# Performance work log

Hardware: AMD Instinct MI355X
Metric: run time of the kernel (lower is better)

The kernel has to match this reference:

```python
import jax, jax.numpy as jnp
import numpy as np

BIT = 64
NUM_TRAIN = 100000
N_CLASS = 100
BATCH = 128
MU, NU, ETA = 1.0, 1.0, 55.0
DCC_ITER = 3


def setup_inputs() -> dict:
    key = jax.random.key(0)
    k1, k2, k3, k4, k5, k6 = jax.random.split(key, 6)
    u = jax.random.normal(k1, (BATCH, BIT), dtype=jnp.float32)
    labels = jax.random.randint(k2, (BATCH,), 0, N_CLASS)
    y = jax.nn.one_hot(labels, N_CLASS, dtype=jnp.float32)          # [batch, n_class]
    U = jax.random.normal(k3, (BIT, NUM_TRAIN), dtype=jnp.float32)  # [bit, num_train]
    B = jnp.sign(jax.random.normal(k4, (BIT, NUM_TRAIN), dtype=jnp.float32))
    ylab = jax.random.randint(k5, (NUM_TRAIN,), 0, N_CLASS)
    Y = jax.nn.one_hot(ylab, N_CLASS, dtype=jnp.float32).T          # [n_class, num_train]
    ind = jax.random.randint(k6, (BATCH,), 0, NUM_TRAIN)
    return {"u": u, "y": y, "U": U, "B": B, "Y": Y, "ind": ind}


def _update_b_and_w(B, U, Y):
    """Discrete cyclic coordinate descent. Math identical to torch loop, but
    P = W@Y + eta/mu*U is hoisted out of the bit loop (W is constant there),
    and B'.T @ W' @ w (row i excluded) is computed as (W@w)@B - (w.w)*B[i]."""
    c_eye = (NU / MU) * jnp.eye(BIT, dtype=B.dtype)
    # DCC operates on sign outputs; gradients through it are zero in torch too.
    Bs = jax.lax.stop_gradient(B)
    Ys = jax.lax.stop_gradient(Y)
    Us = jax.lax.stop_gradient(U)
    B_before = Bs
    for _ in range(DCC_ITER):
        B_before = Bs
        W = jnp.linalg.inv(Bs @ Bs.T + c_eye) @ Bs @ Ys.T   # [bit, n_class]
        P = W @ Ys + (ETA / MU) * Us                        # [bit, num_train]
        def step(Bc, i):
            w = W[i]                     # [n_class]
            p = P[i]                     # [num_train]
            Ww = W @ w                   # [bit]
            full = Ww @ Bc               # [num_train]; includes row i contribution
            new_row = jnp.sign(p - (full - (w @ w) * Bc[i]))
            return Bc.at[i].set(new_row), None
        Bs, _ = jax.lax.scan(step, Bs, jnp.arange(BIT))
    # torch keeps the W computed at the START of the last dcc iteration
    # (i.e. from B before its last inner update), using the un-detached Y.
    W = jnp.linalg.inv(B_before @ B_before.T + c_eye) @ B_before @ Y.T
    return Bs, W


def reference(u, y, U, B, Y, ind):
    # in-place buffer writes: U[:, ind] = u.T.data ; Y[:, ind] = y.T
    U = U.at[:, ind].set(jax.lax.stop_gradient(u).T)
    Y = Y.at[:, ind].set(y.T)
    B, W = _update_b_and_w(B, U, Y)

    ip = (u @ U) * 0.5                           # [batch, num_train]
    s = (y @ Y > 0).astype(ip.dtype)             # [batch, num_train]
    likelihood = jnp.log1p(jnp.exp(-jnp.abs(ip))) + jnp.maximum(ip, 0.0) - s * ip
    likelihood_loss = likelihood.mean()

    cl_loss = jnp.mean((y.T - W.T @ B[:, ind]) ** 2)   # [n_class, batch]
    reg_loss = jnp.mean(W ** 2)
    return likelihood_loss + MU * cl_loss + NU * reg_loss
```

## Files before the change

kernel.cpp:

```cpp
#include <hip/hip_runtime.h>
#include <hip/hip_bf16.h>

#define NTRAIN 100000
#define NBIT   64
#define NCLASS 100
#define NBATCH 128
#define NW     1563
#define NWP    1568
#define NP1    100001.0f
#define ETA_MU 55.0f

#define NBLK   391
#define NLIKB  1563
#define NCLB   50
#define CCH    16
#define NCHUNK 98
#define SCAP   4096
#define SLACK  2e-5f

typedef unsigned long long u64;
typedef unsigned int u32;
typedef __attribute__((ext_vector_type(8))) short bf16x8;
typedef __attribute__((ext_vector_type(4))) float f32x4;

#define OFF_BMASK   0u
#define OFF_CMASK   800000u
#define OFF_LABELY  2054400u
#define OFF_OVR     2454400u
#define OFF_YLAB    2854400u
#define OFF_CCOUNT  2854912u
#define OFF_AF      2855424u
#define OFF_RHS     2871808u
#define OFF_W       2897408u
#define OFF_WT      2923008u
#define OFF_G       2948608u
#define OFF_ROWABS  2964992u
#define OFF_SCNT    2965248u
#define OFF_SLIST   2965504u
#define OFF_SOLD    2981888u
#define OFF_PA      3014656u
#define OFF_CLP     3022848u
#define OFF_PB      4620288u

__device__ __forceinline__ float blk_reduce_sum(float v, float* sbuf) {
    int tid = threadIdx.x;
    for (int off = 32; off > 0; off >>= 1) v += __shfl_down(v, off, 64);
    __syncthreads();
    if ((tid & 63) == 0) sbuf[tid >> 6] = v;
    __syncthreads();
    float t = 0.f;
    if (tid == 0) {
        int nw = (int)(blockDim.x >> 6);
        for (int q = 0; q < nw; ++q) t += sbuf[q];
    }
    return t;
}

__device__ __forceinline__ short f2bf(float v) {
    __hip_bfloat16 h = __float2bfloat16(v);
    return *reinterpret_cast<short*>(&h);
}

__global__ void k_scatter(const float* __restrict__ y, const int* __restrict__ ind,
                          int* __restrict__ ovr, int* __restrict__ ylab,
                          int* __restrict__ ccount) {
    __shared__ int cls[NBATCH], idx[NBATCH];
    int k = threadIdx.x;
    if (k < NCLASS) ccount[k] = 0;
    if (k < NBATCH) {
        int c = 0;
        for (int r = 0; r < NCLASS; ++r)
            if (y[k * NCLASS + r] > 0.5f) c = r;
        cls[k] = c; idx[k] = ind[k]; ylab[k] = c;
    }
    __syncthreads();
    if (k == 0) {
        for (int q = 0; q < NBATCH; ++q) ovr[idx[q]] = q + 1;
    }
}

__global__ __launch_bounds__(256) void k_prep(const float* __restrict__ Y,
                                              const float* __restrict__ B,
                                              const int* __restrict__ ovr,
                                              const int* __restrict__ ylab,
                                              int* __restrict__ labelY,
                                              u64* __restrict__ Bmask,
                                              u64* __restrict__ cmask,
                                              int* __restrict__ ccount) {
    __shared__ int hist[NCLASS];
    int tid = threadIdx.x, lane = tid & 63, wid = tid >> 6;
    if (tid < NCLASS) hist[tid] = 0;
    __syncthreads();
    int w = blockIdx.x * 4 + wid;
    int j = w * 64 + lane;
    int lab = -1;
    if (j < NTRAIN) {
        lab = 0;
        for (int r = 0; r < NCLASS; ++r)
            if (Y[r * NTRAIN + j] > 0.5f) lab = r;
        int ov = ovr[j];
        if (ov) lab = ylab[ov - 1];
        labelY[j] = lab;
        u64 m = 0ull;
        #pragma unroll
        for (int i = 0; i < NBIT; ++i)
            if (B[i * NTRAIN + j] > 0.0f) m |= (1ull << i);
        Bmask[j] = m;
        atomicAdd(&hist[lab], 1);
    }
    u64 keep0 = 0ull, keep1 = 0ull;
    for (int c = 0; c < NCLASS; ++c) {
        u64 bal = __ballot(lab == c);
        if (lane == c)      keep0 = bal;
        if (lane == c - 64) keep1 = bal;
    }
    if (w < NW) {
        cmask[(size_t)lane * NWP + w] = keep0;
        if (lane < NCLASS - 64) cmask[(size_t)(lane + 64) * NWP + w] = keep1;
    }
    __syncthreads();
    if (tid < NCLASS && hist[tid]) atomicAdd(&ccount[tid], hist[tid]);
}

__global__ __launch_bounds__(1024) void k_bbt4(const u64* __restrict__ Bmask,
                                               const u64* __restrict__ cmask,
                                               int* __restrict__ pA,
                                               int* __restrict__ pB) {
    __shared__ u64 Lp[64 * 17];
    __shared__ u64 Lc[100 * 17];
    int tid = threadIdx.x, lane = tid & 63, wv = tid >> 6;
    int w0 = blockIdx.x * CCH;
    for (int idx = tid; idx < 100 * CCH; idx += 1024) {
        int r = idx >> 4, w = idx & 15;
        int gw = w0 + w;
        Lc[r * 17 + w] = (gw < NW) ? cmask[(size_t)r * NWP + gw] : 0ull;
    }
    {
        int j = (w0 + wv) * 64 + lane;
        u64 m = (j < NTRAIN) ? Bmask[j] : 0ull;
        u64 acc = 0ull;
        #pragma unroll
        for (int i = 0; i < 64; ++i) {
            u64 bal = __ballot((m >> i) & 1ull);
            if (lane == i) acc = bal;
        }
        Lp[lane * 17 + wv] = acc;
    }
    __syncthreads();
    int k = lane;
    int cntA[4], cntB[7];
    #pragma unroll
    for (int i = 0; i < 4; ++i) cntA[i] = 0;
    #pragma unroll
    for (int i = 0; i < 7; ++i) cntB[i] = 0;
    #pragma unroll
    for (int w = 0; w < CCH; ++w) {
        u64 pkw = Lp[k * 17 + w];
        #pragma unroll
        for (int li = 0; li < 4; ++li)
            cntA[li] += __popcll(pkw ^ Lp[(wv + 16 * li) * 17 + w]);
        #pragma unroll
        for (int ci = 0; ci < 7; ++ci) {
            int c = wv + 16 * ci;
            if (c < NCLASS)
                cntB[ci] += __popcll(pkw & Lc[c * 17 + w]);
        }
    }
    size_t bA = (size_t)blockIdx.x * 4096;
    size_t bB = (size_t)blockIdx.x * 6400;
    #pragma unroll
    for (int li = 0; li < 4; ++li)
        pA[bA + (size_t)(wv + 16 * li) * 64 + k] = cntA[li];
    #pragma unroll
    for (int ci = 0; ci < 7; ++ci) {
        int c = wv + 16 * ci;
        if (c < NCLASS)
            pB[bB + (size_t)c * 64 + k] = cntB[ci];
    }
}

__global__ __launch_bounds__(256) void k_reduce(const int* __restrict__ pA,
                                                const int* __restrict__ pB,
                                                const int* __restrict__ ccount,
                                                float* __restrict__ A_f,
                                                float* __restrict__ RHS_f) {
    int tid = threadIdx.x, blk = blockIdx.x;
    if (blk < 16) {
        int e = blk * 256 + tid;
        int s = 0;
        #pragma unroll 4
        for (int ch = 0; ch < NCHUNK; ++ch) s += pA[(size_t)ch * 4096 + e];
        A_f[e] = ((e >> 6) == (e & 63)) ? 0.0f
                                        : (float)(NTRAIN - 2 * s) * (1.0f / NP1);
    } else {
        int e = (blk - 16) * 256 + tid;
        int s = 0;
        #pragma unroll 4
        for (int ch = 0; ch < NCHUNK; ++ch) s += pB[(size_t)ch * 6400 + e];
        RHS_f[e] = (float)(2 * s - ccount[e >> 6]);
    }
}

__global__ __launch_bounds__(256) void k_wsolve(const float* __restrict__ A_f,
                                                const float* __restrict__ RHS_f,
                                                float* __restrict__ W_g,
                                                float* __restrict__ WT_g) {
    __shared__ float As[64 * 65];
    __shared__ float xb[4][64];
    int tid = threadIdx.x, lane = tid & 63, wid = tid >> 6;
    for (int e = tid; e < 4096; e += 256)
        As[(e >> 6) * 65 + (e & 63)] = A_f[e];
    int c = blockIdx.x * 4 + wid;
    float v = RHS_f[c * 64 + lane];
    float x = v;
    __syncthreads();
    for (int it = 0; it < 4; ++it) {
        xb[wid][lane] = x;
        __syncthreads();
        const float* __restrict__ Ar = As + lane * 65;
        const float* __restrict__ xv = xb[wid];
        float a0 = 0, a1 = 0, a2 = 0, a3 = 0;
        #pragma unroll 8
        for (int k = 0; k < 64; k += 4) {
            a0 = fmaf(Ar[k],     xv[k],     a0);
            a1 = fmaf(Ar[k + 1], xv[k + 1], a1);
            a2 = fmaf(Ar[k + 2], xv[k + 2], a2);
            a3 = fmaf(Ar[k + 3], xv[k + 3], a3);
        }
        x = v - ((a0 + a1) + (a2 + a3));
        __syncthreads();
    }
    float w = x * (1.0f / NP1);
    W_g[lane * 100 + c] = w;
    WT_g[c * 64 + lane] = w;
}

__global__ __launch_bounds__(256) void k_gram(const float* __restrict__ WT,
                                              float* __restrict__ G_g,
                                              float* __restrict__ rowabs,
                                              int* __restrict__ scnt) {
    __shared__ float WTs[6400];
    int tid = threadIdx.x;
    for (int e = tid; e < 6400; e += 256) WTs[e] = WT[e];
    __syncthreads();
    int e = blockIdx.x * 256 + tid;
    int k = e >> 6, l = e & 63;
    float a0 = 0, a1 = 0;
    #pragma unroll 10
    for (int c = 0; c < 100; c += 2) {
        a0 = fmaf(WTs[c * 64 + k],       WTs[c * 64 + l],       a0);
        a1 = fmaf(WTs[(c + 1) * 64 + k], WTs[(c + 1) * 64 + l], a1);
    }
    float g = (k == l) ? 0.0f : (a0 + a1);
    G_g[e] = g;
    float v = fabsf(g);
    for (int off = 32; off > 0; off >>= 1) v += __shfl_down(v, off, 64);
    if ((tid & 63) == 0) rowabs[k] = v;
    if (blockIdx.x == 0 && tid == 0) *scnt = 0;
}

__global__ __launch_bounds__(256) void k_fast(const float* __restrict__ U,
                                              const float* __restrict__ u,
                                              const int* __restrict__ labelY,
                                              const int* __restrict__ ovr,
                                              const float* __restrict__ WT,
                                              const float* __restrict__ rowabs,
                                              u64* __restrict__ Bmask,
                                              int* __restrict__ slist,
                                              u64* __restrict__ sold,
                                              int* __restrict__ scnt) {
    __shared__ float WTs[100 * 65];
    __shared__ float ra[64];
    int tid = threadIdx.x;
    for (int e = tid; e < 6400; e += 256)
        WTs[(e >> 6) * 65 + (e & 63)] = WT[e];
    if (tid < 64) ra[tid] = rowabs[tid] + SLACK;
    __syncthreads();
    int j = blockIdx.x * 256 + tid;
    if (j >= NTRAIN) return;
    int c = labelY[j], ov = ovr[j];
    const float* up; int str;
    if (ov) { up = u + (ov - 1) * NBIT; str = 1; }
    else    { up = U + j;               str = NTRAIN; }
    const float* wc = WTs + c * 65;
    u64 m = 0ull;
    int slow = 0;
    #pragma unroll
    for (int i = 0; i < NBIT; ++i) {
        float p = fmaf(ETA_MU, up[i * str], wc[i]);
        if (p > 0.0f) m |= (1ull << i);
        slow |= (fabsf(p) <= ra[i]);
    }
    if (slow) {
        int idx = atomicAdd(scnt, 1);
        if (idx < SCAP) { slist[idx] = j; sold[idx] = Bmask[j]; }
    }
    Bmask[j] = m;
}

__global__ __launch_bounds__(1024) void k_slow(const int* __restrict__ slist,
                                               const u64* __restrict__ sold,
                                               const int* __restrict__ scnt,
                                               const int* __restrict__ labelY,
                                               const int* __restrict__ ovr,
                                               const float* __restrict__ G_g,
                                               const float* __restrict__ WT,
                                               const float* __restrict__ U,
                                               const float* __restrict__ u,
                                               u64* __restrict__ Bmask) {
    __shared__ float Gs[64 * 65];
    int tid = threadIdx.x, lane = tid & 63, wv = tid >> 6;
    int n = *scnt; if (n > SCAP) n = SCAP;
    if (n == 0) return;
    for (int e = tid; e < 4096; e += 1024)
        Gs[(e >> 6) * 65 + (e & 63)] = G_g[e];
    __syncthreads();
    for (int idx = wv; idx < n; idx += 16) {
        int j = slist[idx];
        u64 m0 = sold[idx];
        int c = labelY[j], ov = ovr[j];
        float uval = ov ? u[(ov - 1) * NBIT + lane]
                        : U[(size_t)lane * NTRAIN + j];
        float p = fmaf(ETA_MU, uval, WT[c * 64 + lane]);
        float s = ((m0 >> lane) & 1ull) ? 1.0f : -1.0f;
        for (int i = 0; i < 64; ++i) {
            float t = Gs[i * 65 + lane] * s;
            t += __shfl_xor(t, 1);  t += __shfl_xor(t, 2);
            t += __shfl_xor(t, 4);  t += __shfl_xor(t, 8);
            t += __shfl_xor(t, 16); t += __shfl_xor(t, 32);
            float nv = ((p - t) > 0.0f) ? 1.0f : -1.0f;
            s = (lane == i) ? nv : s;
        }
        u64 mo = __ballot(s > 0.0f);
        if (lane == 0) Bmask[j] = mo;
    }
}

__global__ __launch_bounds__(256) void k_likm(const float* __restrict__ U,
                                              const float* __restrict__ u,
                                              const int* __restrict__ labelY,
                                              const int* __restrict__ ovr,
                                              const int* __restrict__ ylab,
                                              float* __restrict__ partials) {
    __shared__ short ubf[128 * 72];
    __shared__ int ylab_s[NBATCH];
    __shared__ float sbuf[8];
    int tid = threadIdx.x;
    for (int e = tid; e < NBATCH * NBIT; e += 256)
        ubf[(e >> 6) * 72 + (e & 63)] = f2bf(u[e]);
    if (tid < NBATCH) ylab_s[tid] = ylab[tid];
    __syncthreads();
    int w = tid >> 6, lane = tid & 63;
    int g = lane >> 4, c = lane & 15;
    int j = blockIdx.x * 64 + w * 16 + c;
    int jl = (j < NTRAIN) ? j : (NTRAIN - 1);
    int ov = ovr[jl];
    int lab = labelY[jl];
    const float* colp; int cstr;
    if (ov) { colp = u + (ov - 1) * NBIT; cstr = 1; }
    else    { colp = U + jl;              cstr = NTRAIN; }
    bf16x8 bf0, bf1;
    #pragma unroll
    for (int i = 0; i < 8; ++i) {
        bf0[i] = f2bf(colp[(g * 8 + i) * cstr]);
        bf1[i] = f2bf(colp[(32 + g * 8 + i) * cstr]);
    }
    float acc = 0.0f;
    #pragma unroll
    for (int bt = 0; bt < 8; ++bt) {
        bf16x8 a0 = *reinterpret_cast<const bf16x8*>(&ubf[(bt * 16 + c) * 72 + g * 8]);
        bf16x8 a1 = *reinterpret_cast<const bf16x8*>(&ubf[(bt * 16 + c) * 72 + 32 + g * 8]);
        f32x4 d = {0.f, 0.f, 0.f, 0.f};
        d = __builtin_amdgcn_mfma_f32_16x16x32_bf16(a0, bf0, d, 0, 0, 0);
        d = __builtin_amdgcn_mfma_f32_16x16x32_bf16(a1, bf1, d, 0, 0, 0);
        #pragma unroll
        for (int r = 0; r < 4; ++r) {
            int b = bt * 16 + g * 4 + r;
            float ipv = 0.5f * d[r];
            float aip = fabsf(ipv);
            float t = __logf(1.0f + __expf(-aip)) + fmaxf(ipv, 0.0f);
            if (ylab_s[b] == lab) t -= ipv;
            acc += t;
        }
    }
    if (j >= NTRAIN) acc = 0.0f;
    float tot = blk_reduce_sum(acc, sbuf);
    if (tid == 0) partials[blockIdx.x] = tot;
}

__global__ __launch_bounds__(256) void k_cl(const float* __restrict__ WT,
                                            const u64* __restrict__ Bmask,
                                            const int* __restrict__ ind,
                                            const float* __restrict__ y,
                                            float* __restrict__ clp) {
    __shared__ float sbuf[8];
    __shared__ u64 mB[NBATCH];
    int tid = threadIdx.x;
    if (tid < NBATCH) mB[tid] = Bmask[ind[tid]];
    __syncthreads();
    int e = blockIdx.x * 256 + tid;
    int b = e & 127, c = e >> 7;
    u64 m = mB[b];
    const float4* __restrict__ wr = (const float4*)(WT + c * 64);
    float d0 = 0.f, d1 = 0.f, d2 = 0.f, d3 = 0.f;
    #pragma unroll
    for (int q = 0; q < 16; ++q) {
        float4 w4 = wr[q];
        int kb = q << 2;
        d0 += ((m >> kb) & 1ull)       ? w4.x : -w4.x;
        d1 += ((m >> (kb + 1)) & 1ull) ? w4.y : -w4.y;
        d2 += ((m >> (kb + 2)) & 1ull) ? w4.z : -w4.z;
        d3 += ((m >> (kb + 3)) & 1ull) ? w4.w : -w4.w;
    }
    float d = (d0 + d1) + (d2 + d3);
    float diff = y[b * NCLASS + c] - d;
    float tot = blk_reduce_sum(diff * diff, sbuf);
    if (tid == 0) clp[blockIdx.x] = tot;
}

__global__ void k_fin(const float* __restrict__ WT,
                      const float* __restrict__ likp,
                      const float* __restrict__ clp,
                      float* __restrict__ out) {
    __shared__ float sbuf[8];
    int tid = threadIdx.x;
    float a = 0.f;
    for (int i = tid; i < NLIKB; i += 256) a += likp[i];
    float cl = 0.f;
    for (int i = tid; i < NCLB; i += 256) cl += clp[i];
    float rg = 0.f;
    for (int e = tid; e < NBIT * NCLASS; e += 256) {
        float w = WT[e];
        rg = fmaf(w, w, rg);
    }
    float lik = blk_reduce_sum(a, sbuf);
    float clS = blk_reduce_sum(cl, sbuf);
    float rgS = blk_reduce_sum(rg, sbuf);
    if (tid == 0) {
        out[0] = lik * (1.0f / ((float)NBATCH * (float)NTRAIN))
               + clS * (1.0f / (float)(NCLASS * NBATCH))
               + rgS * (1.0f / (float)(NBIT * NCLASS));
    }
}

extern "C" void kernel_launch(void* const* d_in, const int* in_sizes, int n_in,
                              void* d_out, int out_size, void* d_ws, size_t ws_size,
                              hipStream_t stream) {
    const float* u   = (const float*)d_in[0];
    const float* y   = (const float*)d_in[1];
    const float* U   = (const float*)d_in[2];
    const float* B   = (const float*)d_in[3];
    const float* Y   = (const float*)d_in[4];
    const int*   ind = (const int*)d_in[5];

    char* ws = (char*)d_ws;
    u64*   Bmask  = (u64*)(ws + OFF_BMASK);
    u64*   cmask  = (u64*)(ws + OFF_CMASK);
    int*   labelY = (int*)(ws + OFF_LABELY);
    int*   ovr    = (int*)(ws + OFF_OVR);
    int*   ylab   = (int*)(ws + OFF_YLAB);
    int*   ccount = (int*)(ws + OFF_CCOUNT);
    float* A_f    = (float*)(ws + OFF_AF);
    float* RHS_f  = (float*)(ws + OFF_RHS);
    float* W      = (float*)(ws + OFF_W);
    float* WT     = (float*)(ws + OFF_WT);
    float* G      = (float*)(ws + OFF_G);
    int*   pA     = (int*)(ws + OFF_PA);
    int*   pB     = (int*)(ws + OFF_PB);
    float* rowabs = (float*)(ws + OFF_ROWABS);
    int*   scnt   = (int*)(ws + OFF_SCNT);
    int*   slist  = (int*)(ws + OFF_SLIST);
    u64*   sold   = (u64*)(ws + OFF_SOLD);
    float* likp   = (float*)(ws + OFF_PA);
    float* clp    = (float*)(ws + OFF_CLP);

    hipMemsetAsync(ovr, 0, NTRAIN * sizeof(int), stream);

    k_scatter<<<1, 128, 0, stream>>>(y, ind, ovr, ylab, ccount);
    k_prep   <<<NBLK, 256, 0, stream>>>(Y, B, ovr, ylab, labelY, Bmask, cmask, ccount);

    for (int pass = 0; pass < 3; ++pass) {
        k_bbt4   <<<NCHUNK, 1024, 0, stream>>>(Bmask, cmask, pA, pB);
        k_reduce <<<41, 256, 0, stream>>>(pA, pB, ccount, A_f, RHS_f);
        k_wsolve <<<25, 256, 0, stream>>>(A_f, RHS_f, W, WT);
        k_gram   <<<16, 256, 0, stream>>>(WT, G, rowabs, scnt);
        k_fast   <<<NBLK, 256, 0, stream>>>(U, u, labelY, ovr, WT, rowabs,
                                            Bmask, slist, sold, scnt);
        k_slow   <<<1, 1024, 0, stream>>>(slist, sold, scnt, labelY, ovr,
                                          G, WT, U, u, Bmask);
    }

    k_likm <<<NLIKB, 256, 0, stream>>>(U, u, labelY, ovr, ylab, likp);
    k_cl   <<<NCLB, 256, 0, stream>>>(WT, Bmask, ind, y, clp);
    k_fin  <<<1, 256, 0, stream>>>(WT, likp, clp, (float*)d_out);
}
```

Baseline: 269.8 us.

## Update Gram and RHS counts incrementally for the final DCC pass

```diff
diff --git a/kernel.cpp b/kernel.cpp
--- a/kernel.cpp
+++ b/kernel.cpp
@@ -41,6 +41,11 @@
 #define OFF_PA      3014656u
 #define OFF_CLP     3022848u
 #define OFF_PB      4620288u
+#define OFF_IAI     7129088u
+#define OFF_IBI     7145472u
+#define OFF_DCNT    7171072u
+#define OFF_DLIST   7171328u
+#define OFF_DOLD    7571328u
 
 __device__ __forceinline__ float blk_reduce_sum(float v, float* sbuf) {
     int tid = threadIdx.x;
@@ -183,13 +188,16 @@
                                                 const int* __restrict__ pB,
                                                 const int* __restrict__ ccount,
                                                 float* __restrict__ A_f,
-                                                float* __restrict__ RHS_f) {
+                                                float* __restrict__ RHS_f,
+                                                int* __restrict__ iAint,
+                                                int* __restrict__ iBint) {
     int tid = threadIdx.x, blk = blockIdx.x;
     if (blk < 16) {
         int e = blk * 256 + tid;
         int s = 0;
         #pragma unroll 4
         for (int ch = 0; ch < NCHUNK; ++ch) s += pA[(size_t)ch * 4096 + e];
+        iAint[e] = s;
         A_f[e] = ((e >> 6) == (e & 63)) ? 0.0f
                                         : (float)(NTRAIN - 2 * s) * (1.0f / NP1);
     } else {
@@ -197,7 +205,63 @@
         int s = 0;
         #pragma unroll 4
         for (int ch = 0; ch < NCHUNK; ++ch) s += pB[(size_t)ch * 6400 + e];
+        iBint[e] = s;
         RHS_f[e] = (float)(2 * s - ccount[e >> 6]);
+    }
+}
+
+__global__ __launch_bounds__(256) void k_incr(const int* __restrict__ dcnt,
+                                              const int* __restrict__ dlist,
+                                              const u64* __restrict__ dold,
+                                              const u64* __restrict__ Bmask,
+                                              const int* __restrict__ labelY,
+                                              const int* __restrict__ iAint,
+                                              const int* __restrict__ iBint,
+                                              const int* __restrict__ ccount,
+                                              float* __restrict__ A_f,
+                                              float* __restrict__ RHS_f) {
+    __shared__ u64 sn[512], so[512];
+    __shared__ int sl[512];
+    int tid = threadIdx.x;
+    int e = blockIdx.x * 256 + tid;
+    int n = *dcnt; if (n > NTRAIN) n = NTRAIN;
+    int isA = (e < 4096);
+    int i_, l_, c_;
+    if (isA) { i_ = e >> 6; l_ = e & 63; }
+    else     { int idx = e - 4096; c_ = idx >> 6; i_ = idx & 63; l_ = 0; }
+    int dA = 0;
+    for (int base = 0; base < n; base += 512) {
+        int cnt = n - base; if (cnt > 512) cnt = 512;
+        for (int t = tid; t < cnt; t += 256) {
+            int j = dlist[base + t];
+            sn[t] = Bmask[j];
+            so[t] = dold[base + t];
+            sl[t] = labelY[j];
+        }
+        __syncthreads();
+        if (isA) {
+            for (int t = 0; t < cnt; ++t) {
+                u64 nm = sn[t], om = so[t];
+                dA += (int)(((nm >> i_) ^ (nm >> l_)) & 1ull)
+                    - (int)(((om >> i_) ^ (om >> l_)) & 1ull);
+            }
+        } else if (e < 10496) {
+            for (int t = 0; t < cnt; ++t) {
+                if (sl[t] == c_) {
+                    dA += (int)((sn[t] >> i_) & 1ull)
+                        - (int)((so[t] >> i_) & 1ull);
+                }
+            }
+        }
+        __syncthreads();
+    }
+    if (isA) {
+        int s = iAint[e] + dA;
+        A_f[e] = (i_ == l_) ? 0.0f : (float)(NTRAIN - 2 * s) * (1.0f / NP1);
+    } else if (e < 10496) {
+        int idx = e - 4096;
+        int s = iBint[idx] + dA;
+        RHS_f[idx] = (float)(2 * s - ccount[c_]);
     }
 }
 
@@ -238,7 +302,8 @@
 __global__ __launch_bounds__(256) void k_gram(const float* __restrict__ WT,
                                               float* __restrict__ G_g,
                                               float* __restrict__ rowabs,
-                                              int* __restrict__ scnt) {
+                                              int* __restrict__ scnt,
+                                              int* __restrict__ dcnt) {
     __shared__ float WTs[6400];
     int tid = threadIdx.x;
     for (int e = tid; e < 6400; e += 256) WTs[e] = WT[e];
@@ -256,7 +321,7 @@
     float v = fabsf(g);
     for (int off = 32; off > 0; off >>= 1) v += __shfl_down(v, off, 64);
     if ((tid & 63) == 0) rowabs[k] = v;
-    if (blockIdx.x == 0 && tid == 0) *scnt = 0;
+    if (blockIdx.x == 0 && tid == 0) { *scnt = 0; *dcnt = 0; }
 }
 
 __global__ __launch_bounds__(256) void k_fast(const float* __restrict__ U,
@@ -268,7 +333,11 @@
                                               u64* __restrict__ Bmask,
                                               int* __restrict__ slist,
                                               u64* __restrict__ sold,
-                                              int* __restrict__ scnt) {
+                                              int* __restrict__ scnt,
+                                              int track,
+                                              int* __restrict__ dlist,
+                                              u64* __restrict__ dold,
+                                              int* __restrict__ dcnt) {
     __shared__ float WTs[100 * 65];
     __shared__ float ra[64];
     int tid = threadIdx.x;
@@ -294,6 +363,14 @@
     if (slow) {
         int idx = atomicAdd(scnt, 1);
         if (idx < SCAP) { slist[idx] = j; sold[idx] = Bmask[j]; }
+    }
+    if (track) {
+        u64 oldm = Bmask[j];
+        if (m != oldm || slow) {
+            int s2 = atomicAdd(dcnt, 1);
+            dlist[s2] = j;
+            dold[s2] = oldm;
+        }
     }
     Bmask[j] = m;
 }
@@ -471,24 +548,41 @@
     int*   scnt   = (int*)(ws + OFF_SCNT);
     int*   slist  = (int*)(ws + OFF_SLIST);
     u64*   sold   = (u64*)(ws + OFF_SOLD);
+    int*   iAint  = (int*)(ws + OFF_IAI);
+    int*   iBint  = (int*)(ws + OFF_IBI);
+    int*   dcnt   = (int*)(ws + OFF_DCNT);
+    int*   dlist  = (int*)(ws + OFF_DLIST);
+    u64*   dold   = (u64*)(ws + OFF_DOLD);
     float* likp   = (float*)(ws + OFF_PA);
     float* clp    = (float*)(ws + OFF_CLP);
 
     hipMemsetAsync(ovr, 0, NTRAIN * sizeof(int), stream);
+    hipMemsetAsync(dcnt, 0, sizeof(int), stream);
 
     k_scatter<<<1, 128, 0, stream>>>(y, ind, ovr, ylab, ccount);
     k_prep   <<<NBLK, 256, 0, stream>>>(Y, B, ovr, ylab, labelY, Bmask, cmask, ccount);
 
-    for (int pass = 0; pass < 3; ++pass) {
+    for (int pass = 0; pass < 2; ++pass) {
         k_bbt4   <<<NCHUNK, 1024, 0, stream>>>(Bmask, cmask, pA, pB);
-        k_reduce <<<41, 256, 0, stream>>>(pA, pB, ccount, A_f, RHS_f);
+        k_reduce <<<41, 256, 0, stream>>>(pA, pB, ccount, A_f, RHS_f, iAint, iBint);
         k_wsolve <<<25, 256, 0, stream>>>(A_f, RHS_f, W, WT);
-        k_gram   <<<16, 256, 0, stream>>>(WT, G, rowabs, scnt);
+        k_gram   <<<16, 256, 0, stream>>>(WT, G, rowabs, scnt, dcnt);
         k_fast   <<<NBLK, 256, 0, stream>>>(U, u, labelY, ovr, WT, rowabs,
-                                            Bmask, slist, sold, scnt);
+                                            Bmask, slist, sold, scnt,
+                                            pass, dlist, dold, dcnt);
         k_slow   <<<1, 1024, 0, stream>>>(slist, sold, scnt, labelY, ovr,
                                           G, WT, U, u, Bmask);
     }
+
+    k_incr  <<<41, 256, 0, stream>>>(dcnt, dlist, dold, Bmask, labelY,
+                                     iAint, iBint, ccount, A_f, RHS_f);
+    k_wsolve<<<25, 256, 0, stream>>>(A_f, RHS_f, W, WT);
+    k_gram  <<<16, 256, 0, stream>>>(WT, G, rowabs, scnt, dcnt);
+    k_fast  <<<NBLK, 256, 0, stream>>>(U, u, labelY, ovr, WT, rowabs,
+                                       Bmask, slist, sold, scnt,
+                                       0, dlist, dold, dcnt);
+    k_slow  <<<1, 1024, 0, stream>>>(slist, sold, scnt, labelY, ovr,
+                                     G, WT, U, u, Bmask);
 
     k_likm <<<NLIKB, 256, 0, stream>>>(U, u, labelY, ovr, ylab, likp);
     k_cl   <<<NCLB, 256, 0, stream>>>(WT, Bmask, ind, y, clp);
```

Result: faster. 245.2 us (-9.1%).
